# Optimization experiments

Measured on AMD Instinct MI355X. Metric: run time of the kernel, lower is better.

## Reference

```python
import jax, jax.numpy as jnp
import numpy as np
from jax import lax

B, T, C = 8, 1024, 1024
H, D = 16, 64          # n_head = n_embd // head_size
NR, NT = 6, 2
E = NR + NT
P = 4                  # bridge max_prefix_len
FF = 4 * C


def _ln(x, g, b):
    m = jnp.mean(x, -1, keepdims=True)
    v = jnp.var(x, -1, keepdims=True)
    return (x - m) * lax.rsqrt(v + 1e-5) * g + b


def setup_inputs() -> dict:
    key = jax.random.key(0)
    ks = jax.random.split(key, 24)
    s = 0.02
    return {
        "x": jax.random.normal(ks[0], (B, T, C), jnp.float32),
        "v_first": jax.random.normal(ks[1], (B, T, C), jnp.float32),
        "capital_shares": jax.random.uniform(ks[2], (E,), jnp.float32),
        "g1": jnp.ones((C,), jnp.float32), "b1": jnp.zeros((C,), jnp.float32),
        "g2": jnp.ones((C,), jnp.float32), "b2": jnp.zeros((C,), jnp.float32),
        "Wr": jax.random.normal(ks[3], (C, C), jnp.float32) * s,
        "Wk": jax.random.normal(ks[4], (C, C), jnp.float32) * s,
        "Wv": jax.random.normal(ks[5], (C, C), jnp.float32) * s,
        "Wo": jax.random.normal(ks[6], (C, C), jnp.float32) * s,
        "w_att": jax.random.normal(ks[7], (H, D), jnp.float32),
        "Wb": jax.random.normal(ks[8], (2 * C, P * C), jnp.float32) * s,
        "Wk_ffn": jax.random.normal(ks[9], (NR, C, FF), jnp.float32) * s,
        "Wv_ffn": jax.random.normal(ks[10], (NR, FF, C), jnp.float32) * s,
        "Wc_rwkv": jax.random.normal(ks[11], (NR, C), jnp.float32) * s,
        "Wq_t": jax.random.normal(ks[12], (NT, C, C), jnp.float32) * s,
        "Wk_t": jax.random.normal(ks[13], (NT, C, C), jnp.float32) * s,
        "Wv_t": jax.random.normal(ks[14], (NT, C, C), jnp.float32) * s,
        "Wo_t": jax.random.normal(ks[15], (NT, C, C), jnp.float32) * s,
        "Wc_trans": jax.random.normal(ks[16], (NT, C), jnp.float32) * s,
        "Wd": jax.random.normal(ks[17], (C,), jnp.float32) * s,
        "Wa": jax.random.normal(ks[18], (C, E), jnp.float32) * s,
    }


def reference(x, v_first, capital_shares, g1, b1, g2, b2, Wr, Wk, Wv, Wo,
              w_att, Wb, Wk_ffn, Wv_ffn, Wc_rwkv, Wq_t, Wk_t, Wv_t, Wo_t,
              Wc_trans, Wd, Wa):
    # ---- attention stage: ln1 + RWKV7-style linear-attn time mix ----
    x_ln = _ln(x, g1, b1)
    r = (x_ln @ Wr).reshape(B, T, H, D)
    k = (x_ln @ Wk).reshape(B, T, H, D)
    v = (x_ln @ Wv).reshape(B, T, H, D)
    decay = jax.nn.sigmoid(w_att)  # per-channel decay in (0,1), [H,D]

    def step(state, inp):
        kt, vt, rt = inp                                   # each [B,H,D]
        state = state * decay[None, :, :, None] + kt[..., None] * vt[..., None, :]
        return state, jnp.einsum('bhd,bhde->bhe', rt, state)

    init = jnp.zeros((B, H, D, D), x.dtype)
    _, outs = lax.scan(step, init, (k.transpose(1, 0, 2, 3),
                                    v.transpose(1, 0, 2, 3),
                                    r.transpose(1, 0, 2, 3)))
    rwkv_state = outs.transpose(1, 0, 2, 3).reshape(B, T, C)
    att_out = rwkv_state @ Wo
    v_first_out = v.reshape(B, T, C)       # layer_id == 0 -> v_first = v
    x_after_att = x + att_out
    h = _ln(x_after_att, g2, b2)

    # ---- routing stage (route_no_grad=True -> fully detached) ----
    rh = lax.stop_gradient(h)
    conf = jnp.concatenate([
        jax.nn.sigmoid(jnp.einsum('btc,ec->bte', rh, Wc_rwkv)),
        jax.nn.sigmoid(jnp.einsum('btc,ec->bte', rh, Wc_trans))], axis=-1)
    difficulty = jax.nn.softplus(rh @ Wd)[..., None]       # [B,T,1]
    affinity = rh @ Wa                                      # [B,T,E]
    subsidy = jax.nn.softmax(affinity, axis=-1)
    bids = conf * lax.stop_gradient(capital_shares) * difficulty + subsidy
    top_vals, winners = lax.top_k(bids, 2)                  # [B,T,2]
    weights = lax.stop_gradient(jax.nn.softmax(top_vals, axis=-1))

    # ---- expert stage: bridge prefix + 8 heterogeneous experts, top-2 mix ----
    prefix = (jnp.concatenate([h, rwkv_state], -1) @ Wb).reshape(B, T, P, C)
    outs_e = []
    for e in range(NR):  # SparseRWKVFFN: relu^2 channel mix
        kk = jnp.square(jax.nn.relu(h @ Wk_ffn[e]))
        outs_e.append(kk @ Wv_ffn[e])
    scale = 1.0 / np.sqrt(D).astype(np.float32)
    for e in range(NT):  # LinearTransformerExpert: cross-attn over bridge prefix
        q = (h @ Wq_t[e]).reshape(B, T, H, D)
        kp = (prefix @ Wk_t[e]).reshape(B, T, P, H, D)
        vp = (prefix @ Wv_t[e]).reshape(B, T, P, H, D)
        att = jax.nn.softmax(jnp.einsum('bthd,btphd->bthp', q, kp) * scale, axis=-1)
        o = jnp.einsum('bthp,btphd->bthd', att, vp).reshape(B, T, C)
        outs_e.append(o @ Wo_t[e])
    expert_outs = jnp.stack(outs_e, axis=2)                 # [B,T,E,C]
    gathered = jnp.take_along_axis(expert_outs, winners[..., None], axis=2)
    final_out = jnp.sum(weights[..., None] * gathered, axis=2)
    return x_after_att + final_out, v_first_out
```

## Files before the change

kernel.cpp:

```cpp
#include <hip/hip_runtime.h>

typedef float f32x4 __attribute__((ext_vector_type(4)));
typedef _Float16 half8 __attribute__((ext_vector_type(8)));

constexpr int kC  = 1024;
constexpr int kFF = 4096;
constexpr size_t MB1 = 1ull << 20;
constexpr long long CB = 8388608ll;

constexpr size_t O_W1H = 0;
constexpr size_t O_W1L = 6*MB1;
constexpr size_t O_WOH = 12*MB1;
constexpr size_t O_WOL = 14*MB1;
constexpr size_t O_WBT = 16*MB1;
constexpr size_t O_WKF = 32*MB1;
constexpr size_t O_WVF = 80*MB1;
constexpr size_t O_WQT = 128*MB1;
constexpr size_t O_WKT = 132*MB1;
constexpr size_t O_WVT = 136*MB1;
constexpr size_t O_WOT = 140*MB1;
constexpr size_t O_XH  = 144*MB1;
constexpr size_t O_XL  = 160*MB1;
constexpr size_t O_RKV = 176*MB1;
constexpr size_t O_RWH = 272*MB1;
constexpr size_t O_RWL = 288*MB1;
constexpr size_t O_AW  = 304*MB1;
constexpr size_t O_CNT = 306*MB1;
constexpr size_t O_OFF = O_CNT + 256;
constexpr size_t O_LTOK = O_CNT + 1024;
constexpr size_t O_LW   = O_LTOK + 8ull*8192*sizeof(int);
constexpr size_t WS_NEED = O_LW + 8ull*8192*sizeof(float) + 1024;

__device__ __forceinline__ void gload16(const _Float16* g, _Float16* l){
  __builtin_amdgcn_global_load_lds(
      (const __attribute__((address_space(1))) void*)g,
      (__attribute__((address_space(3))) void*)l, 16, 0, 0);
}

__device__ __forceinline__ int xcd_swz(int bid, int nwg){
  int q = nwg >> 3, r = nwg & 7;
  int x = bid & 7, i = bid >> 3;
  return (x < r ? x*(q+1) : r*(q+1) + (x-r)*q) + i;
}

__device__ __forceinline__ void decode_mb_nb(int bid, int nNB, int nMB, int dmode,
                                             int& mb, int& nb){
  if (dmode == 0){
    int m8 = bid & 7;
    int t = bid >> 3;
    nb = t % nNB;
    mb = m8 * (nMB >> 3) + t / nNB;
  } else {
    mb = bid % nMB;
    nb = bid / nMB;
  }
}

__global__ void zero_cnt(int* c){ if (threadIdx.x < 8) c[threadIdx.x] = 0; }

__global__ void calc_off(const int* __restrict__ cnt, int* __restrict__ off){
  if (threadIdx.x == 0){
    int s = 0;
    for (int e = 0; e < 6; ++e){ off[e] = s; s += cnt[e]; }
  }
}

__global__ __launch_bounds__(256) void transpose_cvt(
    const float* __restrict__ in, _Float16* __restrict__ outHi,
    _Float16* __restrict__ outLo, int R, int C, float sc1, float sc2,
    int splitR, int split)
{
  __shared__ float tile[32][33];
  size_t zoff = (size_t)blockIdx.z * R * C;
  const float* ip = in + zoff;
  _Float16* oh = outHi + zoff;
  _Float16* ol = outLo ? outLo + zoff : nullptr;
  int c0 = blockIdx.x*32, r0 = blockIdx.y*32;
  int tx = threadIdx.x & 31, ty = threadIdx.x >> 5;
  #pragma unroll
  for (int j = 0; j < 32; j += 8){
    int r = r0+ty+j;
    float s = (r < splitR) ? sc1 : sc2;
    tile[ty+j][tx] = ip[(size_t)r*C + c0+tx] * s;
  }
  __syncthreads();
  #pragma unroll
  for (int j = 0; j < 32; j += 8){
    float v = tile[tx][ty+j];
    _Float16 hi = (_Float16)v;
    oh[(size_t)(c0+ty+j)*R + r0+tx] = hi;
    if (split) ol[(size_t)(c0+ty+j)*R + r0+tx] = (_Float16)(v - (float)hi);
  }
}

__global__ __launch_bounds__(256) void ln_kernel(
    const float* __restrict__ x, const float* __restrict__ g,
    const float* __restrict__ b, float* __restrict__ yF,
    _Float16* __restrict__ yH, _Float16* __restrict__ yHi,
    _Float16* __restrict__ yLo, float fscale)
{
  int row = blockIdx.x, tid = threadIdx.x;
  int lane = tid & 63, wid = tid >> 6;
  __shared__ float red[2][4];
  f32x4 v = ((const f32x4*)(x + (size_t)row*kC))[tid];
  float s = v[0]+v[1]+v[2]+v[3];
  #pragma unroll
  for (int off=32; off; off>>=1) s += __shfl_xor(s, off);
  if (lane==0) red[0][wid] = s;
  __syncthreads();
  float mean = (red[0][0]+red[0][1]+red[0][2]+red[0][3]) * (1.f/1024.f);
  float d0=v[0]-mean, d1=v[1]-mean, d2=v[2]-mean, d3=v[3]-mean;
  float s2 = d0*d0+d1*d1+d2*d2+d3*d3;
  #pragma unroll
  for (int off=32; off; off>>=1) s2 += __shfl_xor(s2, off);
  if (lane==0) red[1][wid] = s2;
  __syncthreads();
  float var = (red[1][0]+red[1][1]+red[1][2]+red[1][3]) * (1.f/1024.f);
  float rs = 1.f / sqrtf(var + 1e-5f);
  f32x4 gg = ((const f32x4*)g)[tid];
  f32x4 bb = ((const f32x4*)b)[tid];
  float y[4];
  y[0] = d0*rs*gg[0]+bb[0];
  y[1] = d1*rs*gg[1]+bb[1];
  y[2] = d2*rs*gg[2]+bb[2];
  y[3] = d3*rs*gg[3]+bb[3];
  size_t base = (size_t)row*kC + tid*4;
  if (yF){
    f32x4 o = {y[0],y[1],y[2],y[3]};
    *(f32x4*)(yF + base) = o;
  }
  if (yH){
    #pragma unroll
    for (int j=0;j<4;j++) yH[base+j] = (_Float16)y[j];
  }
  if (yHi){
    #pragma unroll
    for (int j=0;j<4;j++){
      float ys = y[j]*fscale;
      _Float16 hi = (_Float16)ys;
      yHi[base+j] = hi;
      yLo[base+j] = (_Float16)(ys - (float)hi);
    }
  }
}

template<int ADDX>
__global__ __launch_bounds__(256) void gemm_emu(
    const _Float16* __restrict__ Ah, const _Float16* __restrict__ Al,
    const _Float16* __restrict__ Bh, const _Float16* __restrict__ Bl,
    float* __restrict__ out, const float* __restrict__ addsrc,
    float* __restrict__ vsplit, int M, int N, int K)
{
  __shared__ _Float16 lAh[2][4096], lAl[2][4096], lBh[2][4096], lBl[2][4096];
  int bid = xcd_swz((int)blockIdx.x, (int)gridDim.x);
  int mb, nb;
  decode_mb_nb(bid, N >> 7, M >> 7, 0, mb, nb);
  int tid = threadIdx.x;
  int lane = tid & 63, wid = tid >> 6;
  int wr = wid >> 1, wc = wid & 1;
  int fr = lane & 15, fg = lane >> 4;
  f32x4 z = {0.f,0.f,0.f,0.f};
  f32x4 acc[4][4];
  #pragma unroll
  for (int m=0;m<4;m++)
    #pragma unroll
    for (int n=0;n<4;n++) acc[m][n] = z;

  size_t arow = (size_t)(mb<<7), brow = (size_t)(nb<<7);
  size_t aoff_s[2], boff_s[2]; int ldst_s[2];
  #pragma unroll
  for (int it=0; it<2; ++it){
    int q = (it<<8) + tid;
    int row = q >> 2, c = q & 3;
    int cg = c ^ ((row >> 1) & 3);
    aoff_s[it] = (arow+row)*K + (cg<<3);
    boff_s[it] = (brow+row)*K + (cg<<3);
    ldst_s[it] = q<<3;
  }
  auto STAGE = [&](int buf, int kt){
    #pragma unroll
    for (int it=0; it<2; ++it){
      gload16(Ah + aoff_s[it] + kt, &lAh[buf][ldst_s[it]]);
      gload16(Al + aoff_s[it] + kt, &lAl[buf][ldst_s[it]]);
      gload16(Bh + boff_s[it] + kt, &lBh[buf][ldst_s[it]]);
      gload16(Bl + boff_s[it] + kt, &lBl[buf][ldst_s[it]]);
    }
  };

  STAGE(0, 0);
  __syncthreads();
  int nk = K >> 5, cur = 0;
  for (int ki=0; ki<nk; ++ki){
    if (ki+1 < nk) STAGE(cur^1, (ki+1)<<5);
    half8 ah[4], al[4], bh[4], bl[4];
    #pragma unroll
    for (int m=0;m<4;m++){
      int r = (wr<<6)+(m<<4)+fr;
      int off = (r<<5) + ((fg ^ ((r>>1)&3))<<3);
      ah[m] = *(const half8*)&lAh[cur][off];
      al[m] = *(const half8*)&lAl[cur][off];
    }
    #pragma unroll
    for (int n=0;n<4;n++){
      int r = (wc<<6)+(n<<4)+fr;
      int off = (r<<5) + ((fg ^ ((r>>1)&3))<<3);
      bh[n] = *(const half8*)&lBh[cur][off];
      bl[n] = *(const half8*)&lBl[cur][off];
    }
    #pragma unroll
    for (int m=0;m<4;m++)
      #pragma unroll
      for (int n=0;n<4;n++){
        acc[m][n] = __builtin_amdgcn_mfma_f32_16x16x32_f16(ah[m], bh[n], acc[m][n], 0,0,0);
        acc[m][n] = __builtin_amdgcn_mfma_f32_16x16x32_f16(al[m], bh[n], acc[m][n], 0,0,0);
        acc[m][n] = __builtin_amdgcn_mfma_f32_16x16x32_f16(ah[m], bl[n], acc[m][n], 0,0,0);
      }
    __syncthreads();
    cur ^= 1;
  }
  int m0 = (mb<<7)+(wr<<6), n0 = (nb<<7)+(wc<<6);
  #pragma unroll
  for (int m=0;m<4;m++)
    #pragma unroll
    for (int n=0;n<4;n++)
      #pragma unroll
      for (int i=0;i<4;i++){
        int R = m0+(m<<4)+(fg<<2)+i;
        int Cc = n0+(n<<4)+fr;
        float v = acc[m][n][i] * (1.f/1024.f);
        if (ADDX) v += addsrc[(size_t)R*N + Cc];
        out[(size_t)R*N + Cc] = v;
        if (vsplit && Cc >= 2048) vsplit[(size_t)R*1024 + (Cc-2048)] = v;
      }
}

template<int EPI, int FUSED>
__global__ __launch_bounds__(256) void gemm_h(
    const _Float16* __restrict__ A, const _Float16* __restrict__ A2, int Astride,
    const _Float16* __restrict__ Bw, _Float16* __restrict__ outH,
    float* __restrict__ outF, const int* __restrict__ list,
    const float* __restrict__ listw, const int* __restrict__ cntp,
    int M, int N, int K, int gmode, int cntMul, int Alim, int dmode,
    const int* __restrict__ offp)
{
  if (FUSED){
    int ez = blockIdx.y;
    cntp += ez;
    list += (ez<<13);
    if (listw) listw += (ez<<13);
    Bw += (size_t)ez * (size_t)N * (size_t)K;
    size_t so = (size_t)offp[ez];
    if (EPI == 1) outH += so * (size_t)N;
    if (EPI == 2) A += so * (size_t)Astride;
  }
  int Meff = M;
  if (cntp){ int cv = cntp[0]*cntMul; Meff = cv < M ? cv : M; }
  int nNB = N >> 7;
  int mb, nb;
  if (dmode == 2){
    int nMBa = (Meff + 127) >> 7;
    int T = nMBa * nNB;
    if ((int)blockIdx.x >= T) return;
    int swz = xcd_swz((int)blockIdx.x, T);
    mb = swz / nNB; nb = swz % nNB;
  } else {
    int bid = xcd_swz((int)blockIdx.x, (int)gridDim.x);
    decode_mb_nb(bid, nNB, M >> 7, dmode, mb, nb);
    if ((mb<<7) >= Meff) return;
  }
  __shared__ _Float16 lA[2][8192], lB[2][8192];
  int tid = threadIdx.x;
  int lane = tid & 63, wid = tid >> 6;
  int wr = wid >> 1, wc = wid & 1;
  int fr = lane & 15, fg = lane >> 4;
  f32x4 z = {0.f,0.f,0.f,0.f};
  f32x4 acc[4][4];
  #pragma unroll
  for (int m=0;m<4;m++)
    #pragma unroll
    for (int n=0;n<4;n++) acc[m][n] = z;

  size_t brow = (size_t)(nb<<7);
  int arow_s[4]; size_t boff_s[4]; int kcol_s[4];
  #pragma unroll
  for (int it=0; it<4; ++it){
    int q = (it<<8) + tid;
    int row = q >> 3, c8 = q & 7;
    int c8g = c8 ^ (row & 7);
    int gr = (mb<<7) + row;
    int grc = gr < (M-1) ? gr : (M-1);
    int sr2;
    if (gmode==0) sr2 = gr;
    else if (gmode==1) sr2 = list[grc];
    else sr2 = (list[grc>>2]<<2) + (gr&3);
    sr2 = (sr2 < 0 || sr2 > Alim) ? 0 : sr2;
    arow_s[it] = sr2;
    kcol_s[it] = c8g<<3;
    boff_s[it] = (brow+row)*K + (c8g<<3);
  }

  auto STAGE = [&](int buf, int kt){
    #pragma unroll
    for (int it=0; it<4; ++it){
      int q = (it<<8) + tid;
      int kloc = kt + kcol_s[it];
      const _Float16* asrc;
      if (A2 != nullptr && kloc >= 1024) asrc = A2 + (size_t)arow_s[it]*Astride + (kloc-1024);
      else asrc = A + (size_t)arow_s[it]*Astride + kloc;
      gload16(asrc, &lA[buf][q<<3]);
      gload16(Bw + boff_s[it] + kt, &lB[buf][q<<3]);
    }
  };

  STAGE(0, 0);
  __syncthreads();
  int nk = K >> 6, cur = 0;
  for (int ki=0; ki<nk; ++ki){
    if (ki+1 < nk) STAGE(cur^1, (ki+1)<<6);
    #pragma unroll
    for (int kk2=0; kk2<2; ++kk2){
      int ko8 = (kk2<<2) + fg;
      half8 af[4], bf[4];
      #pragma unroll
      for (int m=0;m<4;m++){
        int r = (wr<<6)+(m<<4)+fr;
        af[m] = *(const half8*)&lA[cur][(r<<6) + ((ko8 ^ (r & 7))<<3)];
      }
      #pragma unroll
      for (int n=0;n<4;n++){
        int r = (wc<<6)+(n<<4)+fr;
        bf[n] = *(const half8*)&lB[cur][(r<<6) + ((ko8 ^ (r & 7))<<3)];
      }
      #pragma unroll
      for (int m=0;m<4;m++)
        #pragma unroll
        for (int n=0;n<4;n++)
          acc[m][n] = __builtin_amdgcn_mfma_f32_16x16x32_f16(af[m], bf[n], acc[m][n], 0,0,0);
    }
    __syncthreads();
    cur ^= 1;
  }
  int m0 = (mb<<7)+(wr<<6), n0 = (nb<<7)+(wc<<6);
  #pragma unroll
  for (int m=0;m<4;m++)
    #pragma unroll
    for (int n=0;n<4;n++)
      #pragma unroll
      for (int i=0;i<4;i++){
        int R = m0+(m<<4)+(fg<<2)+i;
        if (R >= Meff) continue;
        int Cc = n0+(n<<4)+fr;
        float v = acc[m][n][i];
        if (EPI == 0){
          outH[(size_t)R*N + Cc] = (_Float16)v;
        } else if (EPI == 1){
          v = v > 0.f ? v : 0.f;
          outH[(size_t)R*N + Cc] = (_Float16)(v*v);
        } else {
          int tk = list[R];
          float add = listw[R]*v;
          if (FUSED) atomicAdd(&outF[(size_t)tk*N + Cc], add);
          else outF[(size_t)tk*N + Cc] += add;
        }
      }
}

constexpr int SRD = 3072;

__global__ __launch_bounds__(64) void scan_passA(
    const float* __restrict__ rkv, const float* __restrict__ watt,
    float* __restrict__ states)
{
  const float* kb = rkv + 1024;
  const float* vb = rkv + 2048;
  int lane = threadIdx.x, bx = blockIdx.x;
  int chunk = bx & 15, bhq = bx >> 4;
  int b = bhq >> 6, h = (bhq >> 2) & 15, qq = bhq & 3;
  int dg = lane >> 4;
  int e = (qq<<4) + (lane & 15);
  float dec[16];
  #pragma unroll
  for (int i=0;i<16;i++){
    float wv = watt[(h<<6) + (dg<<4) + i];
    dec[i] = 1.f/(1.f + expf(-wv));
  }
  float st[16];
  #pragma unroll
  for (int i=0;i<16;i++) st[i]=0.f;
  __shared__ float sk[64];
  size_t rowbase = ((size_t)(b*1024 + chunk*64))*SRD + (h<<6);
  float pk[4], pv[4];
  #pragma unroll
  for (int j=0;j<4;j++){
    size_t o = rowbase + (size_t)j*SRD;
    pk[j]=kb[o+lane]; pv[j]=vb[o+e];
  }
  for (int t=0;t<64;t+=4){
    #pragma unroll
    for (int s4=0;s4<4;s4++){
      int tt = t+s4;
      sk[lane]=pk[s4];
      float ve = pv[s4];
      __syncthreads();
      if (tt+4 < 64){
        size_t o = rowbase + (size_t)(tt+4)*SRD;
        pk[s4]=kb[o+lane]; pv[s4]=vb[o+e];
      }
      const f32x4* K4 = (const f32x4*)&sk[dg<<4];
      #pragma unroll
      for (int j=0;j<4;j++){
        f32x4 kv = K4[j];
        #pragma unroll
        for (int ii=0;ii<4;ii++){
          int i=(j<<2)+ii;
          st[i] = st[i]*dec[i] + kv[ii]*ve;
        }
      }
      __syncthreads();
    }
  }
  float* sp = states + ((size_t)bhq*16 + chunk)*1024 + (lane<<4);
  #pragma unroll
  for (int i=0;i<16;i++) sp[i] = st[i];
}

__global__ __launch_bounds__(256) void scan_passB(
    float* __restrict__ states, const float* __restrict__ watt)
{
  int bhq = blockIdx.x;
  int h = (bhq >> 2) & 15;
  int t = threadIdx.x;
  int j0 = t*4;
  int d0 = ((j0>>8)<<4) + (j0&15);
  f32x4 wv = *(const f32x4*)(watt + (h<<6) + d0);
  f32x4 dec64;
  #pragma unroll
  for (int j=0;j<4;j++){
    float d = 1.f/(1.f + expf(-wv[j]));
    d = d*d; d = d*d; d = d*d; d = d*d; d = d*d; d = d*d;
    dec64[j] = d;
  }
  f32x4 S = {0.f,0.f,0.f,0.f};
  float* base = states + (size_t)bhq*16*1024 + j0;
  for (int c=0;c<16;c++){
    f32x4 loc = *(f32x4*)(base + (size_t)c*1024);
    *(f32x4*)(base + (size_t)c*1024) = S;
    S = S*dec64 + loc;
  }
}

__global__ __launch_bounds__(64) void scan_passC(
    const float* __restrict__ rkv, const float* __restrict__ watt,
    const float* __restrict__ states,
    _Float16* __restrict__ outHi, _Float16* __restrict__ outLo)
{
  const float* rb = rkv;
  const float* kb = rkv + 1024;
  const float* vb = rkv + 2048;
  int lane = threadIdx.x, bx = blockIdx.x;
  int chunk = bx & 15, bhq = bx >> 4;
  int b = bhq >> 6, h = (bhq >> 2) & 15, qq = bhq & 3;
  int dg = lane >> 4;
  int e = (qq<<4) + (lane & 15);
  float dec[16];
  #pragma unroll
  for (int i=0;i<16;i++){
    float wv = watt[(h<<6) + (dg<<4) + i];
    dec[i] = 1.f/(1.f + expf(-wv));
  }
  float st[16];
  const float* sp = states + ((size_t)bhq*16 + chunk)*1024 + (lane<<4);
  #pragma unroll
  for (int i=0;i<16;i++) st[i] = sp[i];
  __shared__ float sk[64], sr[64];
  size_t rowbase = ((size_t)(b*1024 + chunk*64))*SRD + (h<<6);
  size_t obase   = ((size_t)(b*1024 + chunk*64))*1024 + (h<<6);
  float pk[4], pr[4], pv[4];
  #pragma unroll
  for (int j=0;j<4;j++){
    size_t o = rowbase + (size_t)j*SRD;
    pk[j]=kb[o+lane]; pr[j]=rb[o+lane]; pv[j]=vb[o+e];
  }
  for (int t=0;t<64;t+=4){
    #pragma unroll
    for (int s4=0;s4<4;s4++){
      int tt = t+s4;
      sk[lane]=pk[s4]; sr[lane]=pr[s4];
      float ve = pv[s4];
      __syncthreads();
      if (tt+4 < 64){
        size_t o = rowbase + (size_t)(tt+4)*SRD;
        pk[s4]=kb[o+lane]; pr[s4]=rb[o+lane]; pv[s4]=vb[o+e];
      }
      const f32x4* K4 = (const f32x4*)&sk[dg<<4];
      const f32x4* R4 = (const f32x4*)&sr[dg<<4];
      float p = 0.f;
      #pragma unroll
      for (int j=0;j<4;j++){
        f32x4 kv = K4[j], rv = R4[j];
        #pragma unroll
        for (int ii=0;ii<4;ii++){
          int i=(j<<2)+ii;
          st[i] = st[i]*dec[i] + kv[ii]*ve;
          p += rv[ii]*st[i];
        }
      }
      p += __shfl_xor(p, 16);
      p += __shfl_xor(p, 32);
      if (lane < 16){
        size_t o = obase + (size_t)tt*1024 + (qq<<4) + lane;
        float ps = p*16.f;
        _Float16 hi = (_Float16)ps;
        outHi[o] = hi;
        outLo[o] = (_Float16)(ps - (float)hi);
      }
      __syncthreads();
    }
  }
}

__global__ __launch_bounds__(256) void routing_kernel(
    const float* __restrict__ hf, const float* __restrict__ Wcr,
    const float* __restrict__ Wct, const float* __restrict__ Wd,
    const float* __restrict__ Wa, const float* __restrict__ cap,
    int* __restrict__ cnt, int* __restrict__ listTok, float* __restrict__ listW)
{
  __shared__ int   lt[128];
  __shared__ int   le[128];
  __shared__ float lwv[128];
  int tid = threadIdx.x, wid = tid >> 6, lane = tid & 63;
  float cap8[8];
  #pragma unroll
  for (int e2=0;e2<8;e2++) cap8[e2] = cap[e2];

  for (int tt=0; tt<16; ++tt){
    int t = ((int)blockIdx.x<<6) + (wid<<4) + tt;
    const float* hrow = hf + (size_t)t*kC;
    float hr[16];
    #pragma unroll
    for (int i=0;i<16;i++) hr[i] = hrow[lane + (i<<6)];
    float dots[17];
    #pragma unroll
    for (int e2=0;e2<9;e2++){
      const float* wp = (e2<6) ? (Wcr + (size_t)e2*kC)
                    : (e2<8) ? (Wct + (size_t)(e2-6)*kC) : Wd;
      float a = 0.f;
      #pragma unroll
      for (int i=0;i<16;i++) a += hr[i]*wp[lane+(i<<6)];
      dots[e2] = a;
    }
    #pragma unroll
    for (int e2=0;e2<8;e2++){
      float a = 0.f;
      #pragma unroll
      for (int i=0;i<16;i++) a += hr[i]*Wa[(size_t)(lane+(i<<6))*8 + e2];
      dots[9+e2] = a;
    }
    #pragma unroll
    for (int e2=0;e2<17;e2++){
      float a = dots[e2];
      #pragma unroll
      for (int off=32; off; off>>=1) a += __shfl_xor(a, off);
      dots[e2] = a;
    }
    float diff = dots[8] > 20.f ? dots[8] : log1pf(expf(dots[8]));
    float am = dots[9];
    #pragma unroll
    for (int e2=1;e2<8;e2++) am = fmaxf(am, dots[9+e2]);
    float ee[8]; float es = 0.f;
    #pragma unroll
    for (int e2=0;e2<8;e2++){ ee[e2] = expf(dots[9+e2]-am); es += ee[e2]; }
    float inv = 1.f/es;
    float bids[8];
    #pragma unroll
    for (int e2=0;e2<8;e2++){
      float cf = 1.f/(1.f+expf(-dots[e2]));
      bids[e2] = cf*cap8[e2]*diff + ee[e2]*inv;
    }
    int i0=0; float v0=bids[0];
    #pragma unroll
    for (int e2=1;e2<8;e2++) if (bids[e2]>v0){ v0=bids[e2]; i0=e2; }
    int i1=-1; float v1=-1e30f;
    #pragma unroll
    for (int e2=0;e2<8;e2++) if (e2!=i0 && bids[e2]>v1){ v1=bids[e2]; i1=e2; }
    float x1 = expf(v1-v0);
    float w0 = 1.f/(1.f+x1);
    float w1 = x1/(1.f+x1);
    if (lane==0){
      int slot = (((wid<<4)+tt)<<1);
      lt[slot]   = t; le[slot]   = i0; lwv[slot]   = w0;
      lt[slot+1] = t; le[slot+1] = i1; lwv[slot+1] = w1;
    }
  }
  __syncthreads();
  if (tid < 8){
    int c = 0;
    for (int j=0;j<128;j++) c += (le[j]==tid) ? 1 : 0;
    int b = atomicAdd(&cnt[tid], c);
    for (int j=0;j<128;j++){
      if (le[j]==tid){
        listTok[(tid<<13)+b] = lt[j];
        listW[(tid<<13)+b]  = lwv[j];
        ++b;
      }
    }
  }
}

__global__ __launch_bounds__(256) void attn_logits(
    const _Float16* __restrict__ q, const _Float16* __restrict__ kp,
    float* __restrict__ attw, const int* __restrict__ cntp)
{
  int cnt = cntp[0];
  int gw = ((int)blockIdx.x<<2) + (threadIdx.x>>6);
  int r = gw >> 4, h = gw & 15;
  if (r >= cnt) return;
  int lane = threadIdx.x & 63;
  float qd = (float)q[(size_t)r*kC + (h<<6) + lane];
  float lg[4];
  #pragma unroll
  for (int p=0;p<4;p++){
    float kd = (float)kp[((size_t)(r<<2)+p)*kC + (h<<6) + lane];
    float a = qd*kd;
    #pragma unroll
    for (int off=32; off; off>>=1) a += __shfl_xor(a, off);
    lg[p] = a*0.125f;
  }
  float mx = fmaxf(fmaxf(lg[0],lg[1]),fmaxf(lg[2],lg[3]));
  float ex[4]; float s = 0.f;
  #pragma unroll
  for (int p=0;p<4;p++){ ex[p] = expf(lg[p]-mx); s += ex[p]; }
  float inv = 1.f/s;
  if (lane < 4){
    float pv_ = (lane==0) ? ex[0] : (lane==1) ? ex[1] : (lane==2) ? ex[2] : ex[3];
    attw[((size_t)r<<6) + (h<<2) + lane] = pv_*inv;
  }
}

__global__ __launch_bounds__(256) void attn_av(
    const float* __restrict__ attw, const _Float16* __restrict__ vp,
    _Float16* __restrict__ o, const int* __restrict__ cntp)
{
  int cnt = cntp[0];
  int idx = (int)blockIdx.x*256 + threadIdx.x;
  int r = idx >> 10;
  if (r >= cnt) return;
  int c = idx & 1023; int h = c >> 6;
  const float* aw = attw + ((size_t)r<<6) + (h<<2);
  float s = 0.f;
  #pragma unroll
  for (int p=0;p<4;p++) s += aw[p] * (float)vp[((size_t)(r<<2)+p)*kC + c];
  o[(size_t)r*kC + c] = (_Float16)s;
}

extern "C" void kernel_launch(void* const* d_in, const int* in_sizes, int n_in,
                              void* d_out, int out_size, void* d_ws, size_t ws_size,
                              hipStream_t stream) {
  if (ws_size < WS_NEED) return;
  const float* x    = (const float*)d_in[0];
  const float* cap  = (const float*)d_in[2];
  const float* g1   = (const float*)d_in[3];
  const float* b1   = (const float*)d_in[4];
  const float* g2   = (const float*)d_in[5];
  const float* b2   = (const float*)d_in[6];
  const float* Wr   = (const float*)d_in[7];
  const float* Wk   = (const float*)d_in[8];
  const float* Wv   = (const float*)d_in[9];
  const float* Wo   = (const float*)d_in[10];
  const float* watt = (const float*)d_in[11];
  const float* Wb   = (const float*)d_in[12];
  const float* Wkf  = (const float*)d_in[13];
  const float* Wvf  = (const float*)d_in[14];
  const float* Wcr  = (const float*)d_in[15];
  const float* Wqt  = (const float*)d_in[16];
  const float* Wkt  = (const float*)d_in[17];
  const float* Wvt  = (const float*)d_in[18];
  const float* Wot  = (const float*)d_in[19];
  const float* Wct  = (const float*)d_in[20];
  const float* Wd   = (const float*)d_in[21];
  const float* Wa   = (const float*)d_in[22];

  float* out0 = (float*)d_out;
  float* vout = out0 + CB;
  char* w = (char*)d_ws;
  _Float16* W1h  = (_Float16*)(w+O_W1H);
  _Float16* W1l  = (_Float16*)(w+O_W1L);
  _Float16* WoTh = (_Float16*)(w+O_WOH); _Float16* WoTl = (_Float16*)(w+O_WOL);
  _Float16* WbT  = (_Float16*)(w+O_WBT);
  _Float16* WkfT = (_Float16*)(w+O_WKF);
  _Float16* WvfT = (_Float16*)(w+O_WVF);
  _Float16* WqtT = (_Float16*)(w+O_WQT);
  _Float16* WktT = (_Float16*)(w+O_WKT);
  _Float16* WvtT = (_Float16*)(w+O_WVT);
  _Float16* WotT = (_Float16*)(w+O_WOT);
  _Float16* xlnHi= (_Float16*)(w+O_XH);
  _Float16* xlnLo= (_Float16*)(w+O_XL);
  float*    rkv  = (float*)(w+O_RKV);
  float*    stbuf= (float*)(w+O_XH);
  _Float16* rwHi = (_Float16*)(w+O_RWH);
  _Float16* rwLo = (_Float16*)(w+O_RWL);
  float*    hF   = (float*)(w+O_RKV);
  _Float16* hH   = (_Float16*)(w+O_RWL);
  _Float16* kkpool = (_Float16*)(w+O_XH);
  _Float16* pfxH = (_Float16*)(w+O_RKV+32*MB1);
  _Float16* kpH  = (_Float16*)(w+O_XH);
  _Float16* vpH  = (_Float16*)(w+O_XH);
  _Float16* qH   = (_Float16*)(w+O_RWH);
  _Float16* oH   = (_Float16*)(w+O_RWH);
  float*    attw = (float*)(w+O_AW);
  int*      cnt  = (int*)(w+O_CNT);
  int*      offp = (int*)(w+O_OFF);
  int*   listTok = (int*)(w+O_LTOK);
  float* listW   = (float*)(w+O_LW);

  dim3 TB(256);
  zero_cnt<<<1,64,0,stream>>>(cnt);

  transpose_cvt<<<dim3(32,32,1),TB,0,stream>>>(Wr, W1h,           W1l,           1024,1024, 64.f,64.f,1024, 1);
  transpose_cvt<<<dim3(32,32,1),TB,0,stream>>>(Wk, W1h+1024*1024, W1l+1024*1024, 1024,1024, 64.f,64.f,1024, 1);
  transpose_cvt<<<dim3(32,32,1),TB,0,stream>>>(Wv, W1h+2048*1024, W1l+2048*1024, 1024,1024, 64.f,64.f,1024, 1);
  transpose_cvt<<<dim3(32,32,1),TB,0,stream>>>(Wo, WoTh, WoTl, 1024,1024, 64.f,64.f,1024, 1);
  transpose_cvt<<<dim3(128,64,1),TB,0,stream>>>(Wb,  WbT,  nullptr, 2048,4096, 1.f, 1.f/16.f, 1024, 0);
  transpose_cvt<<<dim3(128,32,6),TB,0,stream>>>(Wkf, WkfT, nullptr, 1024,4096, 1.f,1.f,9999, 0);
  transpose_cvt<<<dim3(32,128,6),TB,0,stream>>>(Wvf, WvfT, nullptr, 4096,1024, 1.f,1.f,9999, 0);
  transpose_cvt<<<dim3(32,32,2),TB,0,stream>>>(Wqt, WqtT, nullptr, 1024,1024, 1.f,1.f,9999, 0);
  transpose_cvt<<<dim3(32,32,2),TB,0,stream>>>(Wkt, WktT, nullptr, 1024,1024, 1.f,1.f,9999, 0);
  transpose_cvt<<<dim3(32,32,2),TB,0,stream>>>(Wvt, WvtT, nullptr, 1024,1024, 1.f,1.f,9999, 0);
  transpose_cvt<<<dim3(32,32,2),TB,0,stream>>>(Wot, WotT, nullptr, 1024,1024, 1.f,1.f,9999, 0);

  ln_kernel<<<8192,TB,0,stream>>>(x, g1, b1, nullptr, nullptr, xlnHi, xlnLo, 16.f);
  gemm_emu<0><<<1536,TB,0,stream>>>(xlnHi, xlnLo, W1h, W1l, rkv, nullptr, vout,
                                    8192, 3072, 1024);
  scan_passA<<<8192,64,0,stream>>>(rkv, watt, stbuf);
  scan_passB<<<512,256,0,stream>>>(stbuf, watt);
  scan_passC<<<8192,64,0,stream>>>(rkv, watt, stbuf, rwHi, rwLo);
  gemm_emu<1><<<512,TB,0,stream>>>(rwHi, rwLo, WoTh, WoTl, out0, x, nullptr,
                                   8192, 1024, 1024);
  ln_kernel<<<8192,TB,0,stream>>>(out0, g2, b2, hF, hH, nullptr, nullptr, 1.f);

  routing_kernel<<<128,TB,0,stream>>>(hF, Wcr, Wct, Wd, Wa, cap, cnt, listTok, listW);
  calc_off<<<1,64,0,stream>>>(cnt, offp);

  gemm_h<1,1><<<dim3(2048,6),TB,0,stream>>>(hH, nullptr, 1024, WkfT, kkpool,
                                  nullptr, listTok, nullptr, cnt,
                                  8192, 4096, 1024, 1, 1, 8191, 2, offp);
  gemm_h<2,1><<<dim3(512,6),TB,0,stream>>>(kkpool, nullptr, 4096, WvfT, nullptr,
                                  out0, listTok, listW, cnt,
                                  8192, 1024, 4096, 0, 1, 8191, 2, offp);

  gemm_h<0,0><<<64*32,TB,0,stream>>>(hH, rwHi, 1024, WbT, pfxH, nullptr,
                                   nullptr, nullptr, nullptr, 8192, 4096, 2048, 0, 1, 8191, 0, nullptr);

  for (int e = 0; e < 2; ++e){
    int ge = 6 + e;
    gemm_h<0,0><<<64*8,TB,0,stream>>>(hH, nullptr, 1024, WqtT + (size_t)e*kC*kC, qH,
                                    nullptr, listTok+ge*8192, nullptr, cnt+ge,
                                    8192, 1024, 1024, 1, 1, 8191, 2, nullptr);
    gemm_h<0,0><<<256*8,TB,0,stream>>>(pfxH, nullptr, 1024, WktT + (size_t)e*kC*kC, kpH,
                                     nullptr, listTok+ge*8192, nullptr, cnt+ge,
                                     32768, 1024, 1024, 2, 4, 32767, 2, nullptr);
    attn_logits<<<32768,TB,0,stream>>>(qH, kpH, attw, cnt+ge);
    gemm_h<0,0><<<256*8,TB,0,stream>>>(pfxH, nullptr, 1024, WvtT + (size_t)e*kC*kC, vpH,
                                     nullptr, listTok+ge*8192, nullptr, cnt+ge,
                                     32768, 1024, 1024, 2, 4, 32767, 2, nullptr);
    attn_av<<<32768,TB,0,stream>>>(attw, vpH, oH, cnt+ge);
    gemm_h<2,0><<<64*8,TB,0,stream>>>(oH, nullptr, 1024, WotT + (size_t)e*kC*kC, nullptr,
                                    out0, listTok+ge*8192, listW+ge*8192, cnt+ge,
                                    8192, 1024, 1024, 0, 1, 8191, 2, nullptr);
  }
}
```

Measured before the change: 1.571 ms.

## Add 256x128-tile triple-buffered fp16 GEMM for expert, bridge and prefix projections

Adds a new gemm_p3 kernel with 512 threads, 256x128 output tiles and a three-stage LDS pipeline gated by explicit vmcnt waits and raw barriers. It replaces gemm_h for the FFN expert GEMMs, the bridge prefix GEMM and the prefix K/V projections. The goal is more reuse of each B tile and deeper latency hiding for global loads. The cost is higher LDS use (about 144 KB per block) and more registers, which lowers occupancy. It also clamps gmode-0 row indices to Meff.

```diff
diff --git a/kernel.cpp b/kernel.cpp
--- a/kernel.cpp
+++ b/kernel.cpp
@@ -290,7 +290,7 @@
     int gr = (mb<<7) + row;
     int grc = gr < (M-1) ? gr : (M-1);
     int sr2;
-    if (gmode==0) sr2 = gr;
+    if (gmode==0) sr2 = gr < (Meff-1) ? gr : (Meff-1);
     else if (gmode==1) sr2 = list[grc];
     else sr2 = (list[grc>>2]<<2) + (gr&3);
     sr2 = (sr2 < 0 || sr2 > Alim) ? 0 : sr2;
@@ -341,6 +341,151 @@
     cur ^= 1;
   }
   int m0 = (mb<<7)+(wr<<6), n0 = (nb<<7)+(wc<<6);
+  #pragma unroll
+  for (int m=0;m<4;m++)
+    #pragma unroll
+    for (int n=0;n<4;n++)
+      #pragma unroll
+      for (int i=0;i<4;i++){
+        int R = m0+(m<<4)+(fg<<2)+i;
+        if (R >= Meff) continue;
+        int Cc = n0+(n<<4)+fr;
+        float v = acc[m][n][i];
+        if (EPI == 0){
+          outH[(size_t)R*N + Cc] = (_Float16)v;
+        } else if (EPI == 1){
+          v = v > 0.f ? v : 0.f;
+          outH[(size_t)R*N + Cc] = (_Float16)(v*v);
+        } else {
+          int tk = list[R];
+          float add = listw[R]*v;
+          if (FUSED) atomicAdd(&outF[(size_t)tk*N + Cc], add);
+          else outF[(size_t)tk*N + Cc] += add;
+        }
+      }
+}
+
+template<int EPI, int FUSED>
+__global__ __launch_bounds__(512) void gemm_p3(
+    const _Float16* __restrict__ A, const _Float16* __restrict__ A2, int Astride,
+    const _Float16* __restrict__ Bw, _Float16* __restrict__ outH,
+    float* __restrict__ outF, const int* __restrict__ list,
+    const float* __restrict__ listw, const int* __restrict__ cntp,
+    int M, int N, int K, int gmode, int cntMul, int Alim,
+    const int* __restrict__ offp)
+{
+  if (FUSED){
+    int ez = blockIdx.y;
+    cntp += ez;
+    list += (ez<<13);
+    if (listw) listw += (ez<<13);
+    Bw += (size_t)ez * (size_t)N * (size_t)K;
+    size_t so = (size_t)offp[ez];
+    if (EPI == 1) outH += so * (size_t)N;
+    if (EPI == 2) A += so * (size_t)Astride;
+  }
+  int Meff = M;
+  if (cntp){ int cv = cntp[0]*cntMul; Meff = cv < M ? cv : M; }
+  int nNB = N >> 7;
+  int nMBa = (Meff + 255) >> 8;
+  int T = nMBa * nNB;
+  if ((int)blockIdx.x >= T) return;
+  int swz = xcd_swz((int)blockIdx.x, T);
+  int mb = swz / nNB, nb = swz % nNB;
+
+  __shared__ _Float16 lA[3][16384];
+  __shared__ _Float16 lB[3][8192];
+
+  int tid = threadIdx.x;
+  int lane = tid & 63, wid = tid >> 6;
+  int wr = wid >> 1, wc = wid & 1;
+  int fr = lane & 15, fg = lane >> 4;
+  f32x4 z = {0.f,0.f,0.f,0.f};
+  f32x4 acc[4][4];
+  #pragma unroll
+  for (int m=0;m<4;m++)
+    #pragma unroll
+    for (int n=0;n<4;n++) acc[m][n] = z;
+
+  int arowA[4]; int kcolA[4];
+  size_t boffB[2];
+  #pragma unroll
+  for (int it=0; it<4; ++it){
+    int q = (it<<9) + tid;
+    int row = q >> 3, c8 = q & 7;
+    int c8g = c8 ^ (row & 7);
+    int gr = (mb<<8) + row;
+    int grc = gr < (M-1) ? gr : (M-1);
+    int sr2;
+    if (gmode==0) sr2 = gr < (Meff-1) ? gr : (Meff-1);
+    else if (gmode==1) sr2 = list[grc];
+    else sr2 = (list[grc>>2]<<2) + (gr&3);
+    sr2 = (sr2 < 0 || sr2 > Alim) ? 0 : sr2;
+    arowA[it] = sr2;
+    kcolA[it] = c8g<<3;
+  }
+  #pragma unroll
+  for (int it=0; it<2; ++it){
+    int q = (it<<9) + tid;
+    int row = q >> 3, c8 = q & 7;
+    int c8g = c8 ^ (row & 7);
+    boffB[it] = ((size_t)(nb<<7)+row)*K + (c8g<<3);
+  }
+
+  auto STAGE = [&](int buf, int kt){
+    #pragma unroll
+    for (int it=0; it<4; ++it){
+      int kloc = kt + kcolA[it];
+      const _Float16* asrc;
+      if (A2 != nullptr && kloc >= 1024) asrc = A2 + (size_t)arowA[it]*Astride + (kloc-1024);
+      else asrc = A + (size_t)arowA[it]*Astride + kloc;
+      gload16(asrc, &lA[buf][((it<<9)+tid)<<3]);
+    }
+    #pragma unroll
+    for (int it=0; it<2; ++it){
+      gload16(Bw + boffB[it] + kt, &lB[buf][((it<<9)+tid)<<3]);
+    }
+  };
+
+  int nk = K >> 6;
+  STAGE(0, 0);
+  if (nk > 1) STAGE(1, 64);
+  if (nk > 2) STAGE(2, 128);
+
+  for (int t=0; t<nk; ++t){
+    int cur = t % 3;
+    if (t+2 < nk)      asm volatile("s_waitcnt vmcnt(12)" ::: "memory");
+    else if (t+1 < nk) asm volatile("s_waitcnt vmcnt(6)"  ::: "memory");
+    else               asm volatile("s_waitcnt vmcnt(0)"  ::: "memory");
+    __builtin_amdgcn_s_barrier();
+    asm volatile("" ::: "memory");
+    #pragma unroll
+    for (int ks=0; ks<2; ++ks){
+      int ko8 = (ks<<2) + fg;
+      half8 af[4], bf[4];
+      #pragma unroll
+      for (int m=0;m<4;m++){
+        int r = (wr<<6)+(m<<4)+fr;
+        af[m] = *(const half8*)&lA[cur][(r<<6) + ((ko8 ^ (r & 7))<<3)];
+      }
+      #pragma unroll
+      for (int n=0;n<4;n++){
+        int r = (wc<<6)+(n<<4)+fr;
+        bf[n] = *(const half8*)&lB[cur][(r<<6) + ((ko8 ^ (r & 7))<<3)];
+      }
+      #pragma unroll
+      for (int m=0;m<4;m++)
+        #pragma unroll
+        for (int n=0;n<4;n++)
+          acc[m][n] = __builtin_amdgcn_mfma_f32_16x16x32_f16(af[m], bf[n], acc[m][n], 0,0,0);
+    }
+    asm volatile("" ::: "memory");
+    __builtin_amdgcn_s_barrier();
+    asm volatile("" ::: "memory");
+    if (t+3 < nk) STAGE(cur, (t+3)<<6);
+  }
+
+  int m0 = (mb<<8)+(wr<<6), n0 = (nb<<7)+(wc<<6);
   #pragma unroll
   for (int m=0;m<4;m++)
     #pragma unroll
@@ -713,7 +858,7 @@
   int*   listTok = (int*)(w+O_LTOK);
   float* listW   = (float*)(w+O_LW);
 
-  dim3 TB(256);
+  dim3 TB(256), TB5(512);
   zero_cnt<<<1,64,0,stream>>>(cnt);
 
   transpose_cvt<<<dim3(32,32,1),TB,0,stream>>>(Wr, W1h,           W1l,           1024,1024, 64.f,64.f,1024, 1);
@@ -741,28 +886,29 @@
   routing_kernel<<<128,TB,0,stream>>>(hF, Wcr, Wct, Wd, Wa, cap, cnt, listTok, listW);
   calc_off<<<1,64,0,stream>>>(cnt, offp);
 
-  gemm_h<1,1><<<dim3(2048,6),TB,0,stream>>>(hH, nullptr, 1024, WkfT, kkpool,
+  gemm_p3<1,1><<<dim3(1024,6),TB5,0,stream>>>(hH, nullptr, 1024, WkfT, kkpool,
                                   nullptr, listTok, nullptr, cnt,
-                                  8192, 4096, 1024, 1, 1, 8191, 2, offp);
-  gemm_h<2,1><<<dim3(512,6),TB,0,stream>>>(kkpool, nullptr, 4096, WvfT, nullptr,
+                                  8192, 4096, 1024, 1, 1, 8191, offp);
+  gemm_p3<2,1><<<dim3(256,6),TB5,0,stream>>>(kkpool, nullptr, 4096, WvfT, nullptr,
                                   out0, listTok, listW, cnt,
-                                  8192, 1024, 4096, 0, 1, 8191, 2, offp);
-
-  gemm_h<0,0><<<64*32,TB,0,stream>>>(hH, rwHi, 1024, WbT, pfxH, nullptr,
-                                   nullptr, nullptr, nullptr, 8192, 4096, 2048, 0, 1, 8191, 0, nullptr);
+                                  8192, 1024, 4096, 0, 1, 8191, offp);
+
+  gemm_p3<0,0><<<dim3(1024),TB5,0,stream>>>(hH, rwHi, 1024, WbT, pfxH, nullptr,
+                                  nullptr, nullptr, nullptr,
+                                  8192, 4096, 2048, 0, 1, 8191, nullptr);
 
   for (int e = 0; e < 2; ++e){
     int ge = 6 + e;
     gemm_h<0,0><<<64*8,TB,0,stream>>>(hH, nullptr, 1024, WqtT + (size_t)e*kC*kC, qH,
                                     nullptr, listTok+ge*8192, nullptr, cnt+ge,
                                     8192, 1024, 1024, 1, 1, 8191, 2, nullptr);
-    gemm_h<0,0><<<256*8,TB,0,stream>>>(pfxH, nullptr, 1024, WktT + (size_t)e*kC*kC, kpH,
-                                     nullptr, listTok+ge*8192, nullptr, cnt+ge,
-                                     32768, 1024, 1024, 2, 4, 32767, 2, nullptr);
+    gemm_p3<0,0><<<dim3(1024),TB5,0,stream>>>(pfxH, nullptr, 1024, WktT + (size_t)e*kC*kC, kpH,
+                                    nullptr, listTok+ge*8192, nullptr, cnt+ge,
+                                    32768, 1024, 1024, 2, 4, 32767, nullptr);
     attn_logits<<<32768,TB,0,stream>>>(qH, kpH, attw, cnt+ge);
-    gemm_h<0,0><<<256*8,TB,0,stream>>>(pfxH, nullptr, 1024, WvtT + (size_t)e*kC*kC, vpH,
-                                     nullptr, listTok+ge*8192, nullptr, cnt+ge,
-                                     32768, 1024, 1024, 2, 4, 32767, 2, nullptr);
+    gemm_p3<0,0><<<dim3(1024),TB5,0,stream>>>(pfxH, nullptr, 1024, WvtT + (size_t)e*kC*kC, vpH,
+                                    nullptr, listTok+ge*8192, nullptr, cnt+ge,
+                                    32768, 1024, 1024, 2, 4, 32767, nullptr);
     attn_av<<<32768,TB,0,stream>>>(attw, vpH, oH, cnt+ge);
     gemm_h<2,0><<<64*8,TB,0,stream>>>(oH, nullptr, 1024, WotT + (size_t)e*kC*kC, nullptr,
                                     out0, listTok+ge*8192, listW+ge*8192, cnt+ge,
```

Measured after the change: 1.632 ms. +3.9%, slower.

## Replace atomic scatter-add in FFN down-projection with staged output and gather combine

Applied to the files above, without the earlier changes.

The fused expert FFN down-projection no longer scatters weighted results into the output with fp32 atomicAdd. It now writes per-expert rows, pre-scaled by their routing weight, in fp16 to a staging buffer. The routing kernel also records each token's position in the expert lists, so a new combine kernel can gather and sum each token's two contributions straight into the output. This removes atomic contention but adds an extra staging write/read pass and fp16 rounding of the expert outputs. The new path only runs when the workspace is at least 340 MB; otherwise the old atomic path is used.

```diff
diff --git a/kernel.cpp b/kernel.cpp
--- a/kernel.cpp
+++ b/kernel.cpp
@@ -29,7 +29,10 @@
 constexpr size_t O_OFF = O_CNT + 256;
 constexpr size_t O_LTOK = O_CNT + 1024;
 constexpr size_t O_LW   = O_LTOK + 8ull*8192*sizeof(int);
-constexpr size_t WS_NEED = O_LW + 8ull*8192*sizeof(float) + 1024;
+constexpr size_t O_INV  = O_LW + 8ull*8192*sizeof(float);
+constexpr size_t WS_NEED = O_INV + 2ull*8192*sizeof(int) + 1024;
+constexpr size_t O_STAGE = 308*MB1;
+constexpr size_t WS_BIG  = 340*MB1;
 
 __device__ __forceinline__ void gload16(const _Float16* g, _Float16* l){
   __builtin_amdgcn_global_load_lds(
@@ -250,8 +253,8 @@
     if (listw) listw += (ez<<13);
     Bw += (size_t)ez * (size_t)N * (size_t)K;
     size_t so = (size_t)offp[ez];
-    if (EPI == 1) outH += so * (size_t)N;
-    if (EPI == 2) A += so * (size_t)Astride;
+    if (EPI == 1 || EPI == 3) outH += so * (size_t)N;
+    if (EPI == 2 || EPI == 3) A += so * (size_t)Astride;
   }
   int Meff = M;
   if (cntp){ int cv = cntp[0]*cntMul; Meff = cv < M ? cv : M; }
@@ -290,7 +293,7 @@
     int gr = (mb<<7) + row;
     int grc = gr < (M-1) ? gr : (M-1);
     int sr2;
-    if (gmode==0) sr2 = gr;
+    if (gmode==0) sr2 = gr < (Meff-1) ? gr : (Meff-1);
     else if (gmode==1) sr2 = list[grc];
     else sr2 = (list[grc>>2]<<2) + (gr&3);
     sr2 = (sr2 < 0 || sr2 > Alim) ? 0 : sr2;
@@ -356,6 +359,8 @@
         } else if (EPI == 1){
           v = v > 0.f ? v : 0.f;
           outH[(size_t)R*N + Cc] = (_Float16)(v*v);
+        } else if (EPI == 3){
+          outH[(size_t)R*N + Cc] = (_Float16)(listw[R]*v);
         } else {
           int tk = list[R];
           float add = listw[R]*v;
@@ -363,6 +368,29 @@
           else outF[(size_t)tk*N + Cc] += add;
         }
       }
+}
+
+__global__ __launch_bounds__(256) void combine_ffn(
+    const int* __restrict__ inv, const int* __restrict__ offp,
+    const _Float16* __restrict__ stage, float* __restrict__ out0)
+{
+  int t = blockIdx.x, tid = threadIdx.x;
+  float acc[4] = {0.f,0.f,0.f,0.f};
+  #pragma unroll
+  for (int s=0; s<2; ++s){
+    int iv = inv[(t<<1)+s];
+    int e = iv >> 13;
+    if (e < 6){
+      int p = iv & 8191;
+      size_t row = (size_t)offp[e] + p;
+      const _Float16* sp = stage + row*1024 + tid*4;
+      #pragma unroll
+      for (int j=0;j<4;j++) acc[j] += (float)sp[j];
+    }
+  }
+  float* op = out0 + (size_t)t*1024 + tid*4;
+  #pragma unroll
+  for (int j=0;j<4;j++) op[j] += acc[j];
 }
 
 constexpr int SRD = 3072;
@@ -523,7 +551,8 @@
     const float* __restrict__ hf, const float* __restrict__ Wcr,
     const float* __restrict__ Wct, const float* __restrict__ Wd,
     const float* __restrict__ Wa, const float* __restrict__ cap,
-    int* __restrict__ cnt, int* __restrict__ listTok, float* __restrict__ listW)
+    int* __restrict__ cnt, int* __restrict__ listTok, float* __restrict__ listW,
+    int* __restrict__ invPos)
 {
   __shared__ int   lt[128];
   __shared__ int   le[128];
@@ -601,6 +630,7 @@
       if (le[j]==tid){
         listTok[(tid<<13)+b] = lt[j];
         listW[(tid<<13)+b]  = lwv[j];
+        invPos[(lt[j]<<1) + (j&1)] = (tid<<13) + b;
         ++b;
       }
     }
@@ -657,6 +687,7 @@
                               void* d_out, int out_size, void* d_ws, size_t ws_size,
                               hipStream_t stream) {
   if (ws_size < WS_NEED) return;
+  const bool bigws = (ws_size >= WS_BIG);
   const float* x    = (const float*)d_in[0];
   const float* cap  = (const float*)d_in[2];
   const float* g1   = (const float*)d_in[3];
@@ -712,6 +743,8 @@
   int*      offp = (int*)(w+O_OFF);
   int*   listTok = (int*)(w+O_LTOK);
   float* listW   = (float*)(w+O_LW);
+  int*   invPos  = (int*)(w+O_INV);
+  _Float16* stageH = (_Float16*)(w+O_STAGE);
 
   dim3 TB(256);
   zero_cnt<<<1,64,0,stream>>>(cnt);
@@ -738,15 +771,22 @@
                                    8192, 1024, 1024);
   ln_kernel<<<8192,TB,0,stream>>>(out0, g2, b2, hF, hH, nullptr, nullptr, 1.f);
 
-  routing_kernel<<<128,TB,0,stream>>>(hF, Wcr, Wct, Wd, Wa, cap, cnt, listTok, listW);
+  routing_kernel<<<128,TB,0,stream>>>(hF, Wcr, Wct, Wd, Wa, cap, cnt, listTok, listW, invPos);
   calc_off<<<1,64,0,stream>>>(cnt, offp);
 
   gemm_h<1,1><<<dim3(2048,6),TB,0,stream>>>(hH, nullptr, 1024, WkfT, kkpool,
                                   nullptr, listTok, nullptr, cnt,
                                   8192, 4096, 1024, 1, 1, 8191, 2, offp);
-  gemm_h<2,1><<<dim3(512,6),TB,0,stream>>>(kkpool, nullptr, 4096, WvfT, nullptr,
-                                  out0, listTok, listW, cnt,
-                                  8192, 1024, 4096, 0, 1, 8191, 2, offp);
+  if (bigws){
+    gemm_h<3,1><<<dim3(512,6),TB,0,stream>>>(kkpool, nullptr, 4096, WvfT, stageH,
+                                    nullptr, listTok, listW, cnt,
+                                    8192, 1024, 4096, 0, 1, 8191, 2, offp);
+    combine_ffn<<<8192,TB,0,stream>>>(invPos, offp, stageH, out0);
+  } else {
+    gemm_h<2,1><<<dim3(512,6),TB,0,stream>>>(kkpool, nullptr, 4096, WvfT, nullptr,
+                                    out0, listTok, listW, cnt,
+                                    8192, 1024, 4096, 0, 1, 8191, 2, offp);
+  }
 
   gemm_h<0,0><<<64*32,TB,0,stream>>>(hH, rwHi, 1024, WbT, pfxH, nullptr,
                                    nullptr, nullptr, nullptr, 8192, 4096, 2048, 0, 1, 8191, 0, nullptr);
```

New measurement: 1.541 ms. Within noise of the previous version (-1.9%).
